# Kernel optimization log

Measured on AMD Instinct MI355X. Metric: run time of the kernel, lower is better.

The kernel has to match this reference:

```python
import jax, jax.numpy as jnp
import numpy as np

EPS = 1e-5

def conv1d(x, w, b):
    # Keras Conv1D, channels_last, padding='same'. x: [B,L,Cin], w: [K,Cin,Cout]
    y = jax.lax.conv_general_dilated(x, w, window_strides=(1,), padding='SAME',
                                     dimension_numbers=('NWC', 'WIO', 'NWC'))
    return y + b

def rmsnorm(x, w):
    return x * jax.lax.rsqrt(jnp.mean(jnp.square(x), axis=-1, keepdims=True) + EPS) * w

def setup_inputs() -> dict:
    key = jax.random.key(0)
    ks = jax.random.split(key, 12)
    B, L, D, S = 4, 4096, 512, 16
    D2 = 2 * D
    def w(k, shape, scale=0.02):
        return (jax.random.normal(k, shape, jnp.float32) * scale)
    return {
        'x': jax.random.normal(ks[0], (B, L, D), jnp.float32),
        'norm_w': jnp.ones((D,), jnp.float32),
        'inp_w': w(ks[1], (3, D, D2)),  'inp_b': jnp.zeros((D2,), jnp.float32),
        'conv_w': w(ks[2], (3, D2, D2)), 'conv_b': jnp.zeros((D2,), jnp.float32),
        'cl_w': w(ks[3], (3, D2, D2)),   'cl_b': jnp.zeros((D2,), jnp.float32),
        'fc1_w': w(ks[4], (3, D2, D2)),  'fc1_b': jnp.zeros((D2,), jnp.float32),
        'fc2_w': w(ks[5], (3, D2, S)),   'fc2_b': jnp.zeros((S,), jnp.float32),
        'fc3_w': w(ks[6], (3, D2, S)),   'fc3_b': jnp.zeros((S,), jnp.float32),
        'A': w(ks[7], (D2, S), 0.1),
        'res_w': w(ks[8], (3, D, D2)),   'res_b': jnp.zeros((D2,), jnp.float32),
        'out_w': w(ks[9], (3, D2, D)),   'out_b': jnpp if False else jnp.zeros((D,), jnp.float32),
    }

def s6(x, fc1_w, fc1_b, fc2_w, fc2_b, fc3_w, fc3_b, A):
    # Original: dB = delta[...,None]*B[:,:,None,:]; dA = exp(delta[...,None]*A);
    # h = dA * zeros + x[...,None] * dB  ==  x[...,None] * dB  (dA term is exactly 0)
    # y = einsum('bln,bldn->bld', C, h) = x * delta * sum_n(C*B)
    Bm = conv1d(x, fc2_w, fc2_b)            # [B,L,n]
    Cm = conv1d(x, fc3_w, fc3_b)            # [B,L,n]
    delta = jax.nn.softplus(conv1d(x, fc1_w, fc1_b))  # [B,L,2d]
    cb = jnp.einsum('bln,bln->bl', Cm, Bm)  # [B,L]
    return x * delta * cb[..., None]        # [B,L,2d]

def reference(x, norm_w, inp_w, inp_b, conv_w, conv_b, cl_w, cl_b,
              fc1_w, fc1_b, fc2_w, fc2_b, fc3_w, fc3_b, A,
              res_w, res_b, out_w, out_b):
    xn = rmsnorm(x, norm_w)
    x_proj = conv1d(xn, inp_w, inp_b)
    x_conv = jax.nn.swish(conv1d(x_proj, conv_w, conv_b))
    x_conv_out = conv1d(x_conv, cl_w, cl_b)
    x_ssm = s6(x_conv_out, fc1_w, fc1_b, fc2_w, fc2_b, fc3_w, fc3_b, A)
    x_res = jax.nn.swish(conv1d(xn, res_w, res_b))
    return conv1d(x_ssm * x_res, out_w, out_b)
```

## Files before the change

### kernel.cpp

```cpp
#include <hip/hip_runtime.h>
#include <hip/hip_fp16.h>

typedef _Float16 f16;
typedef _Float16 half8  __attribute__((ext_vector_type(8)));
typedef _Float16 half4v __attribute__((ext_vector_type(4)));
typedef _Float16 half2v __attribute__((ext_vector_type(2)));
typedef float    floatx4 __attribute__((ext_vector_type(4)));

constexpr int SEQ  = 4096;
constexpr int SEQP = 4098;

__device__ __forceinline__ void dma16(const void* g, char* ldsBase, unsigned off) {
  __builtin_amdgcn_global_load_lds(
      (const __attribute__((address_space(1))) void*)g,
      (__attribute__((address_space(3))) void*)(ldsBase + off),
      16, 0, 0);
}

template <int EPI>
__global__ __launch_bounds__(256, 2)
void gemm_k(const f16* __restrict__ A, const f16* __restrict__ Wt,
            const float* __restrict__ bias, void* __restrict__ Cp,
            int K, int lda, long batchStrideA,
            int ldc, long batchStrideC, int rowOff)
{
  __shared__ f16 lds[8192];
  char* ldsB = (char*)lds;

  const int tid  = threadIdx.x;
  const int lane = tid & 63;
  const int wv   = tid >> 6;
  const int quad = lane >> 4;
  const int lr   = lane & 15;
  const int w_row = wv >> 1, w_col = wv & 1;

  const int r0 = blockIdx.x * 128;
  const int n0 = blockIdx.y * 128;
  const int b  = r0 >> 12;
  const int l0 = r0 & (SEQ - 1);

  const f16* Ab = A + (long)b * batchStrideA + (long)l0 * lda;

  const int c0 = tid, c1 = tid + 256;
  const f16* gA0 = Ab + (long)(c0 >> 2) * lda + (c0 & 3) * 8;
  const f16* gA1 = Ab + (long)(c1 >> 2) * lda + (c1 & 3) * 8;
  const f16* gB0 = Wt + (long)(n0 + (c0 >> 2)) * K + (c0 & 3) * 8;
  const f16* gB1 = Wt + (long)(n0 + (c1 >> 2)) * K + (c1 & 3) * 8;
  const unsigned la0 = wv * 1024;
  const unsigned la1 = 4096  + wv * 1024;
  const unsigned lb0 = 8192  + wv * 1024;
  const unsigned lb1 = 12288 + wv * 1024;

  floatx4 acc[4][4];
#pragma unroll
  for (int mi = 0; mi < 4; mi++)
#pragma unroll
    for (int ni = 0; ni < 4; ni++) acc[mi][ni] = (floatx4){0.f, 0.f, 0.f, 0.f};

  for (int k0 = 0; k0 < K; k0 += 32) {
    __syncthreads();
    dma16(gA0 + k0, ldsB, la0);
    dma16(gA1 + k0, ldsB, la1);
    dma16(gB0 + k0, ldsB, lb0);
    dma16(gB1 + k0, ldsB, lb1);
    __syncthreads();

    half8 af[4], bf[4];
#pragma unroll
    for (int mi = 0; mi < 4; mi++)
      af[mi] = *(const half8*)&lds[(w_row * 64 + mi * 16 + lr) * 32 + quad * 8];
#pragma unroll
    for (int ni = 0; ni < 4; ni++)
      bf[ni] = *(const half8*)&lds[4096 + (w_col * 64 + ni * 16 + lr) * 32 + quad * 8];

#pragma unroll
    for (int mi = 0; mi < 4; mi++)
#pragma unroll
      for (int ni = 0; ni < 4; ni++)
        acc[mi][ni] = __builtin_amdgcn_mfma_f32_16x16x32_f16(af[mi], bf[ni], acc[mi][ni], 0, 0, 0);
  }

  const int colBase = n0 + w_col * 64 + lr;
  float bv[4];
#pragma unroll
  for (int ni = 0; ni < 4; ni++) bv[ni] = bias[colBase + ni * 16];

  const long cbb = (long)b * batchStrideC;
#pragma unroll
  for (int mi = 0; mi < 4; mi++) {
#pragma unroll
    for (int i = 0; i < 4; i++) {
      const int rl = w_row * 64 + mi * 16 + quad * 4 + i;
      const long rowFlat = cbb + (long)(l0 + rl + rowOff) * ldc;
#pragma unroll
      for (int ni = 0; ni < 4; ni++) {
        float v = acc[mi][ni][i] + bv[ni];
        if (EPI == 1) v = v / (1.f + expf(-v));
        if (EPI == 2) ((float*)Cp)[rowFlat + colBase + ni * 16] = v;
        else          ((f16*)Cp)[rowFlat + colBase + ni * 16] = (f16)v;
      }
    }
  }
}

__global__ __launch_bounds__(256)
void wt_transpose(const float* __restrict__ w, f16* __restrict__ wt, int K, int N)
{
  __shared__ float tile[32][33];
  const int kt = blockIdx.x * 32, nt = blockIdx.y * 32;
  const int tx = threadIdx.x & 31, ty = threadIdx.x >> 5;
#pragma unroll
  for (int i = 0; i < 32; i += 8)
    tile[ty + i][tx] = w[(long)(kt + ty + i) * N + nt + tx];
  __syncthreads();
#pragma unroll
  for (int i = 0; i < 32; i += 8)
    wt[(long)(nt + ty + i) * K + kt + tx] = (f16)tile[tx][ty + i];
}

__global__ void fc23_build(const float* __restrict__ fc2, const float* __restrict__ fc3,
                           f16* __restrict__ wt)
{
  int idx = blockIdx.x * 256 + threadIdx.x;
  int n = idx / 3072, k = idx - n * 3072;
  float v = 0.f;
  if (n < 16)      v = fc2[k * 16 + n];
  else if (n < 32) v = fc3[k * 16 + n - 16];
  wt[idx] = (f16)v;
}

__global__ void fc23_bias(const float* __restrict__ b2, const float* __restrict__ b3,
                          float* __restrict__ bo)
{
  int t = threadIdx.x;
  if (t < 128) bo[t] = t < 16 ? b2[t] : (t < 32 ? b3[t - 16] : 0.f);
}

__global__ void zero_pads(f16* xn, f16* xproj, f16* xconv, f16* xco)
{
  int b = blockIdx.x >> 1, e = blockIdx.x & 1;
  f16* base; int C;
  switch (blockIdx.y) {
    case 0:  base = xn;    C = 512;  break;
    case 1:  base = xproj; C = 1024; break;
    case 2:  base = xconv; C = 1024; break;
    default: base = xco;   C = 1024; break;
  }
  long p = e ? (SEQP - 1) : 0;
  f16* row = base + ((long)b * SEQP + p) * C;
  for (int c = threadIdx.x; c < C; c += 256) row[c] = (f16)0;
}

__global__ __launch_bounds__(256)
void rmsnorm_k(const float* __restrict__ x, const float* __restrict__ nw,
               f16* __restrict__ xn)
{
  const int row = blockIdx.x;
  const int b = row >> 12, l = row & (SEQ - 1);
  const int t = threadIdx.x;
  float2 v = ((const float2*)(x + (long)row * 512))[t];
  float ss = v.x * v.x + v.y * v.y;
#pragma unroll
  for (int o = 32; o > 0; o >>= 1) ss += __shfl_down(ss, o, 64);
  __shared__ float sred[4];
  if ((t & 63) == 0) sred[t >> 6] = ss;
  __syncthreads();
  float tot = sred[0] + sred[1] + sred[2] + sred[3];
  float rs = rsqrtf(tot * (1.f / 512.f) + 1e-5f);
  float2 w = ((const float2*)nw)[t];
  half2v o2;
  o2.x = (f16)(v.x * rs * w.x);
  o2.y = (f16)(v.y * rs * w.y);
  ((half2v*)(xn + ((long)b * SEQP + l + 1) * 512))[t] = o2;
}

__global__ __launch_bounds__(256)
void combine_k(const f16* __restrict__ delta_pre, const f16* __restrict__ xco_pad,
               const f16* __restrict__ bmcm, const f16* __restrict__ xres,
               f16* __restrict__ prod_pad)
{
  const int row = blockIdx.x;
  const int b = row >> 12, l = row & (SEQ - 1);
  const int t = threadIdx.x;
  __shared__ float cb_s;
  if (t < 16) {
    float bmv = (float)bmcm[(long)row * 128 + t];
    float cmv = (float)bmcm[(long)row * 128 + 16 + t];
    float p = bmv * cmv;
#pragma unroll
    for (int o = 8; o > 0; o >>= 1) p += __shfl_down(p, o, 64);
    if (t == 0) cb_s = p;
  }
  __syncthreads();
  const float cb = cb_s;
  const long urow = (long)row * 1024;
  const long prow = ((long)b * SEQP + l + 1) * 1024;
  half4v dp = ((const half4v*)(delta_pre + urow))[t];
  half4v xc = ((const half4v*)(xco_pad + prow))[t];
  half4v xr = ((const half4v*)(xres + urow))[t];
  half4v o;
#pragma unroll
  for (int j = 0; j < 4; j++) {
    float d  = (float)dp[j];
    float sp = d > 20.f ? d : log1pf(expf(d));
    o[j] = (f16)((float)xc[j] * sp * cb * (float)xr[j]);
  }
  ((half4v*)(prod_pad + prow))[t] = o;
}

extern "C" void kernel_launch(void* const* d_in, const int* in_sizes, int n_in,
                              void* d_out, int out_size, void* d_ws, size_t ws_size,
                              hipStream_t stream)
{
  const float* x      = (const float*)d_in[0];
  const float* norm_w = (const float*)d_in[1];
  const float* inp_w  = (const float*)d_in[2];
  const float* inp_b  = (const float*)d_in[3];
  const float* conv_w = (const float*)d_in[4];
  const float* conv_b = (const float*)d_in[5];
  const float* cl_w   = (const float*)d_in[6];
  const float* cl_b   = (const float*)d_in[7];
  const float* fc1_w  = (const float*)d_in[8];
  const float* fc1_b  = (const float*)d_in[9];
  const float* fc2_w  = (const float*)d_in[10];
  const float* fc2_b  = (const float*)d_in[11];
  const float* fc3_w  = (const float*)d_in[12];
  const float* fc3_b  = (const float*)d_in[13];
  const float* res_w  = (const float*)d_in[15];
  const float* res_b  = (const float*)d_in[16];
  const float* out_w  = (const float*)d_in[17];
  const float* out_b  = (const float*)d_in[18];

  char* ws = (char*)d_ws;
  size_t off = 0;
  auto alloc = [&](size_t bytes) -> char* {
    char* p = ws + off; off += (bytes + 511) & ~(size_t)511; return p;
  };
  f16* Wt_inp   = (f16*)alloc(1024ull * 1536 * 2);
  f16* Wt_conv  = (f16*)alloc(1024ull * 3072 * 2);
  f16* Wt_cl    = (f16*)alloc(1024ull * 3072 * 2);
  f16* Wt_fc1   = (f16*)alloc(1024ull * 3072 * 2);
  f16* Wt_fc23  = (f16*)alloc(128ull  * 3072 * 2);
  f16* Wt_res   = (f16*)alloc(1024ull * 1536 * 2);
  f16* Wt_out   = (f16*)alloc(512ull  * 3072 * 2);
  float* b_fc23 = (float*)alloc(128 * 4);
  f16* xn_pad    = (f16*)alloc(4ull * SEQP * 512  * 2);
  f16* xproj_pad = (f16*)alloc(4ull * SEQP * 1024 * 2);
  f16* xconv_pad = (f16*)alloc(4ull * SEQP * 1024 * 2);
  f16* xco_pad   = (f16*)alloc(4ull * SEQP * 1024 * 2);
  f16* bmcm      = (f16*)alloc(16384ull * 128  * 2);
  f16* xres      = (f16*)alloc(16384ull * 1024 * 2);

  wt_transpose<<<dim3(1536 / 32, 1024 / 32), 256, 0, stream>>>(inp_w,  Wt_inp,  1536, 1024);
  wt_transpose<<<dim3(3072 / 32, 1024 / 32), 256, 0, stream>>>(conv_w, Wt_conv, 3072, 1024);
  wt_transpose<<<dim3(3072 / 32, 1024 / 32), 256, 0, stream>>>(cl_w,   Wt_cl,   3072, 1024);
  wt_transpose<<<dim3(3072 / 32, 1024 / 32), 256, 0, stream>>>(fc1_w,  Wt_fc1,  3072, 1024);
  wt_transpose<<<dim3(1536 / 32, 1024 / 32), 256, 0, stream>>>(res_w,  Wt_res,  1536, 1024);
  wt_transpose<<<dim3(3072 / 32,  512 / 32), 256, 0, stream>>>(out_w,  Wt_out,  3072, 512);
  fc23_build<<<1536, 256, 0, stream>>>(fc2_w, fc3_w, Wt_fc23);
  fc23_bias<<<1, 128, 0, stream>>>(fc2_b, fc3_b, b_fc23);
  zero_pads<<<dim3(8, 4), 256, 0, stream>>>(xn_pad, xproj_pad, xconv_pad, xco_pad);

  rmsnorm_k<<<16384, 256, 0, stream>>>(x, norm_w, xn_pad);

  gemm_k<0><<<dim3(128, 8), 256, 0, stream>>>(xn_pad, Wt_inp, inp_b, xproj_pad,
      1536, 512, (long)SEQP * 512, 1024, (long)SEQP * 1024, 1);
  gemm_k<1><<<dim3(128, 8), 256, 0, stream>>>(xproj_pad, Wt_conv, conv_b, xconv_pad,
      3072, 1024, (long)SEQP * 1024, 1024, (long)SEQP * 1024, 1);
  gemm_k<0><<<dim3(128, 8), 256, 0, stream>>>(xconv_pad, Wt_cl, cl_b, xco_pad,
      3072, 1024, (long)SEQP * 1024, 1024, (long)SEQP * 1024, 1);
  f16* delta_pre = xconv_pad;
  gemm_k<0><<<dim3(128, 8), 256, 0, stream>>>(xco_pad, Wt_fc1, fc1_b, delta_pre,
      3072, 1024, (long)SEQP * 1024, 1024, (long)SEQ * 1024, 0);
  gemm_k<0><<<dim3(128, 1), 256, 0, stream>>>(xco_pad, Wt_fc23, b_fc23, bmcm,
      3072, 1024, (long)SEQP * 1024, 128, (long)SEQ * 128, 0);
  gemm_k<1><<<dim3(128, 8), 256, 0, stream>>>(xn_pad, Wt_res, res_b, xres,
      1536, 512, (long)SEQP * 512, 1024, (long)SEQ * 1024, 0);
  f16* prod_pad = xproj_pad;
  combine_k<<<16384, 256, 0, stream>>>(delta_pre, xco_pad, bmcm, xres, prod_pad);
  gemm_k<2><<<dim3(128, 4), 256, 0, stream>>>(prod_pad, Wt_out, out_b, d_out,
      3072, 1024, (long)SEQP * 1024, 512, (long)SEQ * 512, 0);
}
```

Baseline: 858.7 us.

## Fuse combine into res GEMM epilogue, merge fc1/fc23 GEMMs, swizzle LDS

```diff
diff --git a/kernel.cpp b/kernel.cpp
--- a/kernel.cpp
+++ b/kernel.cpp
@@ -3,7 +3,6 @@
 
 typedef _Float16 f16;
 typedef _Float16 half8  __attribute__((ext_vector_type(8)));
-typedef _Float16 half4v __attribute__((ext_vector_type(4)));
 typedef _Float16 half2v __attribute__((ext_vector_type(2)));
 typedef float    floatx4 __attribute__((ext_vector_type(4)));
 
@@ -21,6 +20,8 @@
 __global__ __launch_bounds__(256, 2)
 void gemm_k(const f16* __restrict__ A, const f16* __restrict__ Wt,
             const float* __restrict__ bias, void* __restrict__ Cp,
+            void* __restrict__ Cp2, const f16* __restrict__ Edelta,
+            const f16* __restrict__ Exco, const float* __restrict__ Ecb,
             int K, int lda, long batchStrideA,
             int ldc, long batchStrideC, int rowOff)
 {
@@ -41,11 +42,13 @@
 
   const f16* Ab = A + (long)b * batchStrideA + (long)l0 * lda;
 
-  const int c0 = tid, c1 = tid + 256;
-  const f16* gA0 = Ab + (long)(c0 >> 2) * lda + (c0 & 3) * 8;
-  const f16* gA1 = Ab + (long)(c1 >> 2) * lda + (c1 & 3) * 8;
-  const f16* gB0 = Wt + (long)(n0 + (c0 >> 2)) * K + (c0 & 3) * 8;
-  const f16* gB1 = Wt + (long)(n0 + (c1 >> 2)) * K + (c1 & 3) * 8;
+  const int s0 = tid, s1 = tid + 256;
+  const int r0s = s0 >> 2, c0s = ((s0 & 3) ^ ((s0 >> 3) & 3)) * 8;
+  const int r1s = s1 >> 2, c1s = ((s1 & 3) ^ ((s1 >> 3) & 3)) * 8;
+  const f16* gA0 = Ab + (long)r0s * lda + c0s;
+  const f16* gA1 = Ab + (long)r1s * lda + c1s;
+  const f16* gB0 = Wt + (long)(n0 + r0s) * K + c0s;
+  const f16* gB1 = Wt + (long)(n0 + r1s) * K + c1s;
   const unsigned la0 = wv * 1024;
   const unsigned la1 = 4096  + wv * 1024;
   const unsigned lb0 = 8192  + wv * 1024;
@@ -56,6 +59,8 @@
   for (int mi = 0; mi < 4; mi++)
 #pragma unroll
     for (int ni = 0; ni < 4; ni++) acc[mi][ni] = (floatx4){0.f, 0.f, 0.f, 0.f};
+
+  const int swz = (quad ^ ((lr >> 1) & 3)) * 8;
 
   for (int k0 = 0; k0 < K; k0 += 32) {
     __syncthreads();
@@ -68,10 +73,10 @@
     half8 af[4], bf[4];
 #pragma unroll
     for (int mi = 0; mi < 4; mi++)
-      af[mi] = *(const half8*)&lds[(w_row * 64 + mi * 16 + lr) * 32 + quad * 8];
+      af[mi] = *(const half8*)&lds[(w_row * 64 + mi * 16 + lr) * 32 + swz];
 #pragma unroll
     for (int ni = 0; ni < 4; ni++)
-      bf[ni] = *(const half8*)&lds[4096 + (w_col * 64 + ni * 16 + lr) * 32 + quad * 8];
+      bf[ni] = *(const half8*)&lds[4096 + (w_col * 64 + ni * 16 + lr) * 32 + swz];
 
 #pragma unroll
     for (int mi = 0; mi < 4; mi++)
@@ -92,30 +97,62 @@
     for (int i = 0; i < 4; i++) {
       const int rl = w_row * 64 + mi * 16 + quad * 4 + i;
       const long rowFlat = cbb + (long)(l0 + rl + rowOff) * ldc;
+      const int rg = r0 + rl;
 #pragma unroll
       for (int ni = 0; ni < 4; ni++) {
+        const int c = colBase + ni * 16;
         float v = acc[mi][ni][i] + bv[ni];
-        if (EPI == 1) v = v / (1.f + expf(-v));
-        if (EPI == 2) ((float*)Cp)[rowFlat + colBase + ni * 16] = v;
-        else          ((f16*)Cp)[rowFlat + colBase + ni * 16] = (f16)v;
+        if (EPI == 0) {
+          ((f16*)Cp)[rowFlat + c] = (f16)v;
+        } else if (EPI == 1) {
+          v = v / (1.f + expf(-v));
+          ((f16*)Cp)[rowFlat + c] = (f16)v;
+        } else if (EPI == 2) {
+          ((float*)Cp)[rowFlat + c] = v;
+        } else if (EPI == 3) {
+          v = v / (1.f + expf(-v));
+          float d  = (float)Edelta[(long)rg * 1024 + c];
+          float sp = d > 20.f ? d : log1pf(expf(d));
+          float xc = (float)Exco[rowFlat + c];
+          ((f16*)Cp)[rowFlat + c] = (f16)(xc * sp * Ecb[rg] * v);
+        } else {
+          if (c < 1024)      ((f16*)Cp)[rowFlat + c] = (f16)v;
+          else if (c < 1056) ((f16*)Cp2)[(long)rg * 32 + (c - 1024)] = (f16)v;
+        }
       }
     }
   }
 }
 
 __global__ __launch_bounds__(256)
-void wt_transpose(const float* __restrict__ w, f16* __restrict__ wt, int K, int N)
-{
+void wt_all(const float* __restrict__ s0, const float* __restrict__ s1,
+            const float* __restrict__ s2, const float* __restrict__ s3,
+            const float* __restrict__ s4, const float* __restrict__ s5,
+            f16* d0, f16* d1, f16* d2, f16* d3, f16* d4, f16* d5)
+{
+  const float* src; f16* dst; int K, N;
+  switch (blockIdx.y) {
+    case 0:  src = s0; dst = d0; K = 1536; N = 1024; break;
+    case 1:  src = s1; dst = d1; K = 3072; N = 1024; break;
+    case 2:  src = s2; dst = d2; K = 3072; N = 1024; break;
+    case 3:  src = s3; dst = d3; K = 3072; N = 1024; break;
+    case 4:  src = s4; dst = d4; K = 1536; N = 1024; break;
+    default: src = s5; dst = d5; K = 3072; N = 512;  break;
+  }
+  const int ktiles = K >> 5;
+  const int t = blockIdx.x;
+  if (t >= ktiles * (N >> 5)) return;
+  const int kt = (t % ktiles) * 32, nt = (t / ktiles) * 32;
+
   __shared__ float tile[32][33];
-  const int kt = blockIdx.x * 32, nt = blockIdx.y * 32;
   const int tx = threadIdx.x & 31, ty = threadIdx.x >> 5;
 #pragma unroll
   for (int i = 0; i < 32; i += 8)
-    tile[ty + i][tx] = w[(long)(kt + ty + i) * N + nt + tx];
+    tile[ty + i][tx] = src[(long)(kt + ty + i) * N + nt + tx];
   __syncthreads();
 #pragma unroll
   for (int i = 0; i < 32; i += 8)
-    wt[(long)(nt + ty + i) * K + kt + tx] = (f16)tile[tx][ty + i];
+    dst[(long)(nt + ty + i) * K + kt + tx] = (f16)tile[tx][ty + i];
 }
 
 __global__ void fc23_build(const float* __restrict__ fc2, const float* __restrict__ fc3,
@@ -129,11 +166,16 @@
   wt[idx] = (f16)v;
 }
 
-__global__ void fc23_bias(const float* __restrict__ b2, const float* __restrict__ b3,
-                          float* __restrict__ bo)
-{
-  int t = threadIdx.x;
-  if (t < 128) bo[t] = t < 16 ? b2[t] : (t < 32 ? b3[t - 16] : 0.f);
+__global__ void bias_build(const float* __restrict__ b1, const float* __restrict__ b2,
+                           const float* __restrict__ b3, float* __restrict__ bo)
+{
+  int t = blockIdx.x * 256 + threadIdx.x;
+  if (t >= 1152) return;
+  float v = 0.f;
+  if (t < 1024)      v = b1[t];
+  else if (t < 1040) v = b2[t - 1024];
+  else if (t < 1056) v = b3[t - 1040];
+  bo[t] = v;
 }
 
 __global__ void zero_pads(f16* xn, f16* xproj, f16* xconv, f16* xco)
@@ -175,37 +217,16 @@
 }
 
 __global__ __launch_bounds__(256)
-void combine_k(const f16* __restrict__ delta_pre, const f16* __restrict__ xco_pad,
-               const f16* __restrict__ bmcm, const f16* __restrict__ xres,
-               f16* __restrict__ prod_pad)
-{
-  const int row = blockIdx.x;
-  const int b = row >> 12, l = row & (SEQ - 1);
-  const int t = threadIdx.x;
-  __shared__ float cb_s;
-  if (t < 16) {
-    float bmv = (float)bmcm[(long)row * 128 + t];
-    float cmv = (float)bmcm[(long)row * 128 + 16 + t];
-    float p = bmv * cmv;
-#pragma unroll
-    for (int o = 8; o > 0; o >>= 1) p += __shfl_down(p, o, 64);
-    if (t == 0) cb_s = p;
-  }
-  __syncthreads();
-  const float cb = cb_s;
-  const long urow = (long)row * 1024;
-  const long prow = ((long)b * SEQP + l + 1) * 1024;
-  half4v dp = ((const half4v*)(delta_pre + urow))[t];
-  half4v xc = ((const half4v*)(xco_pad + prow))[t];
-  half4v xr = ((const half4v*)(xres + urow))[t];
-  half4v o;
-#pragma unroll
-  for (int j = 0; j < 4; j++) {
-    float d  = (float)dp[j];
-    float sp = d > 20.f ? d : log1pf(expf(d));
-    o[j] = (f16)((float)xc[j] * sp * cb * (float)xr[j]);
-  }
-  ((half4v*)(prod_pad + prow))[t] = o;
+void cb_k(const f16* __restrict__ bmcm, float* __restrict__ cb)
+{
+  int r = blockIdx.x * 256 + threadIdx.x;
+  const half8* p = (const half8*)(bmcm + (long)r * 32);
+  half8 b0 = p[0], b1 = p[1], c0 = p[2], c1 = p[3];
+  float s = 0.f;
+#pragma unroll
+  for (int j = 0; j < 8; j++)
+    s += (float)b0[j] * (float)c0[j] + (float)b1[j] * (float)c1[j];
+  cb[r] = s;
 }
 
 extern "C" void kernel_launch(void* const* d_in, const int* in_sizes, int n_in,
@@ -239,45 +260,44 @@
   f16* Wt_inp   = (f16*)alloc(1024ull * 1536 * 2);
   f16* Wt_conv  = (f16*)alloc(1024ull * 3072 * 2);
   f16* Wt_cl    = (f16*)alloc(1024ull * 3072 * 2);
-  f16* Wt_fc1   = (f16*)alloc(1024ull * 3072 * 2);
-  f16* Wt_fc23  = (f16*)alloc(128ull  * 3072 * 2);
+  f16* Wt_fc1x  = (f16*)alloc(1152ull * 3072 * 2);
   f16* Wt_res   = (f16*)alloc(1024ull * 1536 * 2);
   f16* Wt_out   = (f16*)alloc(512ull  * 3072 * 2);
-  float* b_fc23 = (float*)alloc(128 * 4);
+  float* b_fc1x = (float*)alloc(1152 * 4);
   f16* xn_pad    = (f16*)alloc(4ull * SEQP * 512  * 2);
   f16* xproj_pad = (f16*)alloc(4ull * SEQP * 1024 * 2);
   f16* xconv_pad = (f16*)alloc(4ull * SEQP * 1024 * 2);
   f16* xco_pad   = (f16*)alloc(4ull * SEQP * 1024 * 2);
-  f16* bmcm      = (f16*)alloc(16384ull * 128  * 2);
-  f16* xres      = (f16*)alloc(16384ull * 1024 * 2);
-
-  wt_transpose<<<dim3(1536 / 32, 1024 / 32), 256, 0, stream>>>(inp_w,  Wt_inp,  1536, 1024);
-  wt_transpose<<<dim3(3072 / 32, 1024 / 32), 256, 0, stream>>>(conv_w, Wt_conv, 3072, 1024);
-  wt_transpose<<<dim3(3072 / 32, 1024 / 32), 256, 0, stream>>>(cl_w,   Wt_cl,   3072, 1024);
-  wt_transpose<<<dim3(3072 / 32, 1024 / 32), 256, 0, stream>>>(fc1_w,  Wt_fc1,  3072, 1024);
-  wt_transpose<<<dim3(1536 / 32, 1024 / 32), 256, 0, stream>>>(res_w,  Wt_res,  1536, 1024);
-  wt_transpose<<<dim3(3072 / 32,  512 / 32), 256, 0, stream>>>(out_w,  Wt_out,  3072, 512);
-  fc23_build<<<1536, 256, 0, stream>>>(fc2_w, fc3_w, Wt_fc23);
-  fc23_bias<<<1, 128, 0, stream>>>(fc2_b, fc3_b, b_fc23);
+  f16* bmcm      = (f16*)alloc(16384ull * 32 * 2);
+  float* cb      = (float*)alloc(16384ull * 4);
+
+  wt_all<<<dim3(3072, 6), 256, 0, stream>>>(inp_w, conv_w, cl_w, fc1_w, res_w, out_w,
+                                            Wt_inp, Wt_conv, Wt_cl, Wt_fc1x, Wt_res, Wt_out);
+  fc23_build<<<1536, 256, 0, stream>>>(fc2_w, fc3_w, Wt_fc1x + 1024ull * 3072);
+  bias_build<<<5, 256, 0, stream>>>(fc1_b, fc2_b, fc3_b, b_fc1x);
   zero_pads<<<dim3(8, 4), 256, 0, stream>>>(xn_pad, xproj_pad, xconv_pad, xco_pad);
 
   rmsnorm_k<<<16384, 256, 0, stream>>>(x, norm_w, xn_pad);
 
   gemm_k<0><<<dim3(128, 8), 256, 0, stream>>>(xn_pad, Wt_inp, inp_b, xproj_pad,
+      nullptr, nullptr, nullptr, nullptr,
       1536, 512, (long)SEQP * 512, 1024, (long)SEQP * 1024, 1);
   gemm_k<1><<<dim3(128, 8), 256, 0, stream>>>(xproj_pad, Wt_conv, conv_b, xconv_pad,
+      nullptr, nullptr, nullptr, nullptr,
       3072, 1024, (long)SEQP * 1024, 1024, (long)SEQP * 1024, 1);
   gemm_k<0><<<dim3(128, 8), 256, 0, stream>>>(xconv_pad, Wt_cl, cl_b, xco_pad,
+      nullptr, nullptr, nullptr, nullptr,
       3072, 1024, (long)SEQP * 1024, 1024, (long)SEQP * 1024, 1);
   f16* delta_pre = xconv_pad;
-  gemm_k<0><<<dim3(128, 8), 256, 0, stream>>>(xco_pad, Wt_fc1, fc1_b, delta_pre,
+  gemm_k<4><<<dim3(128, 9), 256, 0, stream>>>(xco_pad, Wt_fc1x, b_fc1x, delta_pre,
+      bmcm, nullptr, nullptr, nullptr,
       3072, 1024, (long)SEQP * 1024, 1024, (long)SEQ * 1024, 0);
-  gemm_k<0><<<dim3(128, 1), 256, 0, stream>>>(xco_pad, Wt_fc23, b_fc23, bmcm,
-      3072, 1024, (long)SEQP * 1024, 128, (long)SEQ * 128, 0);
-  gemm_k<1><<<dim3(128, 8), 256, 0, stream>>>(xn_pad, Wt_res, res_b, xres,
-      1536, 512, (long)SEQP * 512, 1024, (long)SEQ * 1024, 0);
+  cb_k<<<64, 256, 0, stream>>>(bmcm, cb);
   f16* prod_pad = xproj_pad;
-  combine_k<<<16384, 256, 0, stream>>>(delta_pre, xco_pad, bmcm, xres, prod_pad);
+  gemm_k<3><<<dim3(128, 8), 256, 0, stream>>>(xn_pad, Wt_res, res_b, prod_pad,
+      nullptr, delta_pre, xco_pad, cb,
+      1536, 512, (long)SEQP * 512, 1024, (long)SEQP * 1024, 1);
   gemm_k<2><<<dim3(128, 4), 256, 0, stream>>>(prod_pad, Wt_out, out_b, d_out,
+      nullptr, nullptr, nullptr, nullptr,
       3072, 1024, (long)SEQP * 1024, 512, (long)SEQ * 512, 0);
 }
```

Result: no change. 863.7 us (+0.6%).

## Deepen GEMM K-step with swizzled LDS, merge inp/res GEMMs, split-K fc23

Applied to the files above, without the earlier changes.

```diff
diff --git a/kernel.cpp b/kernel.cpp
--- a/kernel.cpp
+++ b/kernel.cpp
@@ -21,10 +21,11 @@
 __global__ __launch_bounds__(256, 2)
 void gemm_k(const f16* __restrict__ A, const f16* __restrict__ Wt,
             const float* __restrict__ bias, void* __restrict__ Cp,
-            int K, int lda, long batchStrideA,
-            int ldc, long batchStrideC, int rowOff)
-{
-  __shared__ f16 lds[8192];
+            void* __restrict__ Cp2,
+            int kSlice, int lda, long bsA, int ldb,
+            int ldc, long bsC, int rowOff)
+{
+  __shared__ f16 lds[16384];
   char* ldsB = (char*)lds;
 
   const int tid  = threadIdx.x;
@@ -38,18 +39,13 @@
   const int n0 = blockIdx.y * 128;
   const int b  = r0 >> 12;
   const int l0 = r0 & (SEQ - 1);
-
-  const f16* Ab = A + (long)b * batchStrideA + (long)l0 * lda;
-
-  const int c0 = tid, c1 = tid + 256;
-  const f16* gA0 = Ab + (long)(c0 >> 2) * lda + (c0 & 3) * 8;
-  const f16* gA1 = Ab + (long)(c1 >> 2) * lda + (c1 & 3) * 8;
-  const f16* gB0 = Wt + (long)(n0 + (c0 >> 2)) * K + (c0 & 3) * 8;
-  const f16* gB1 = Wt + (long)(n0 + (c1 >> 2)) * K + (c1 & 3) * 8;
-  const unsigned la0 = wv * 1024;
-  const unsigned la1 = 4096  + wv * 1024;
-  const unsigned lb0 = 8192  + wv * 1024;
-  const unsigned lb1 = 12288 + wv * 1024;
+  const int kBeg = blockIdx.z * kSlice;
+
+  const int trow   = tid >> 3;
+  const int tchunk = ((tid & 7) ^ ((tid >> 3) & 7)) * 8;
+  const f16* gA = A + (long)b * bsA + (long)(l0 + trow) * lda + kBeg + tchunk;
+  const f16* gB = Wt + (long)(n0 + trow) * ldb + kBeg + tchunk;
+  const long stepA = 32l * lda, stepB = 32l * ldb;
 
   floatx4 acc[4][4];
 #pragma unroll
@@ -57,65 +53,104 @@
 #pragma unroll
     for (int ni = 0; ni < 4; ni++) acc[mi][ni] = (floatx4){0.f, 0.f, 0.f, 0.f};
 
-  for (int k0 = 0; k0 < K; k0 += 32) {
+  const int colx = (quad ^ (lr & 7)) * 8;
+
+  for (int k0 = 0; k0 < kSlice; k0 += 64) {
     __syncthreads();
-    dma16(gA0 + k0, ldsB, la0);
-    dma16(gA1 + k0, ldsB, la1);
-    dma16(gB0 + k0, ldsB, lb0);
-    dma16(gB1 + k0, ldsB, lb1);
+#pragma unroll
+    for (int j = 0; j < 4; j++) {
+      dma16(gA + k0 + j * stepA, ldsB,         j * 4096 + wv * 1024);
+      dma16(gB + k0 + j * stepB, ldsB, 16384 + j * 4096 + wv * 1024);
+    }
     __syncthreads();
 
-    half8 af[4], bf[4];
-#pragma unroll
-    for (int mi = 0; mi < 4; mi++)
-      af[mi] = *(const half8*)&lds[(w_row * 64 + mi * 16 + lr) * 32 + quad * 8];
-#pragma unroll
-    for (int ni = 0; ni < 4; ni++)
-      bf[ni] = *(const half8*)&lds[4096 + (w_col * 64 + ni * 16 + lr) * 32 + quad * 8];
-
-#pragma unroll
-    for (int mi = 0; mi < 4; mi++)
+#pragma unroll
+    for (int s = 0; s < 2; s++) {
+      const int cs = colx ^ (s * 32);
+      half8 af[4], bf[4];
+#pragma unroll
+      for (int mi = 0; mi < 4; mi++)
+        af[mi] = *(const half8*)&lds[(w_row * 64 + mi * 16 + lr) * 64 + cs];
 #pragma unroll
       for (int ni = 0; ni < 4; ni++)
-        acc[mi][ni] = __builtin_amdgcn_mfma_f32_16x16x32_f16(af[mi], bf[ni], acc[mi][ni], 0, 0, 0);
+        bf[ni] = *(const half8*)&lds[8192 + (w_col * 64 + ni * 16 + lr) * 64 + cs];
+#pragma unroll
+      for (int mi = 0; mi < 4; mi++)
+#pragma unroll
+        for (int ni = 0; ni < 4; ni++)
+          acc[mi][ni] = __builtin_amdgcn_mfma_f32_16x16x32_f16(af[mi], bf[ni], acc[mi][ni], 0, 0, 0);
+    }
   }
 
   const int colBase = n0 + w_col * 64 + lr;
   float bv[4];
 #pragma unroll
-  for (int ni = 0; ni < 4; ni++) bv[ni] = bias[colBase + ni * 16];
-
-  const long cbb = (long)b * batchStrideC;
+  for (int ni = 0; ni < 4; ni++)
+    bv[ni] = (EPI == 6 && blockIdx.z != 0) ? 0.f : bias[colBase + ni * 16];
+
+  const long cbb = (long)b * bsC;
 #pragma unroll
   for (int mi = 0; mi < 4; mi++) {
 #pragma unroll
     for (int i = 0; i < 4; i++) {
       const int rl = w_row * 64 + mi * 16 + quad * 4 + i;
       const long rowFlat = cbb + (long)(l0 + rl + rowOff) * ldc;
+      const int rg = r0 + rl;
 #pragma unroll
       for (int ni = 0; ni < 4; ni++) {
+        const int c = colBase + ni * 16;
         float v = acc[mi][ni][i] + bv[ni];
-        if (EPI == 1) v = v / (1.f + expf(-v));
-        if (EPI == 2) ((float*)Cp)[rowFlat + colBase + ni * 16] = v;
-        else          ((f16*)Cp)[rowFlat + colBase + ni * 16] = (f16)v;
+        if (EPI == 0) {
+          ((f16*)Cp)[rowFlat + c] = (f16)v;
+        } else if (EPI == 1) {
+          v = v / (1.f + expf(-v));
+          ((f16*)Cp)[rowFlat + c] = (f16)v;
+        } else if (EPI == 2) {
+          ((float*)Cp)[rowFlat + c] = v;
+        } else if (EPI == 5) {
+          if (c < 1024) {
+            ((f16*)Cp)[cbb + (long)(l0 + rl + 1) * 1024 + c] = (f16)v;
+          } else {
+            v = v / (1.f + expf(-v));
+            ((f16*)Cp2)[(long)rg * 1024 + (c - 1024)] = (f16)v;
+          }
+        } else {
+          if (c < 32) atomicAdd((float*)Cp + (long)rg * 32 + c, v);
+        }
       }
     }
   }
 }
 
 __global__ __launch_bounds__(256)
-void wt_transpose(const float* __restrict__ w, f16* __restrict__ wt, int K, int N)
-{
+void wt_all(const float* __restrict__ s0, const float* __restrict__ s1,
+            const float* __restrict__ s2, const float* __restrict__ s3,
+            const float* __restrict__ s4, const float* __restrict__ s5,
+            f16* d0, f16* d1, f16* d2, f16* d3, f16* d4, f16* d5)
+{
+  const float* src; f16* dst; int K, N;
+  switch (blockIdx.y) {
+    case 0:  src = s0; dst = d0; K = 1536; N = 1024; break;
+    case 1:  src = s1; dst = d1; K = 3072; N = 1024; break;
+    case 2:  src = s2; dst = d2; K = 3072; N = 1024; break;
+    case 3:  src = s3; dst = d3; K = 3072; N = 1024; break;
+    case 4:  src = s4; dst = d4; K = 1536; N = 1024; break;
+    default: src = s5; dst = d5; K = 3072; N = 512;  break;
+  }
+  const int ktiles = K >> 5;
+  const int t = blockIdx.x;
+  if (t >= ktiles * (N >> 5)) return;
+  const int kt = (t % ktiles) * 32, nt = (t / ktiles) * 32;
+
   __shared__ float tile[32][33];
-  const int kt = blockIdx.x * 32, nt = blockIdx.y * 32;
   const int tx = threadIdx.x & 31, ty = threadIdx.x >> 5;
 #pragma unroll
   for (int i = 0; i < 32; i += 8)
-    tile[ty + i][tx] = w[(long)(kt + ty + i) * N + nt + tx];
+    tile[ty + i][tx] = src[(long)(kt + ty + i) * N + nt + tx];
   __syncthreads();
 #pragma unroll
   for (int i = 0; i < 32; i += 8)
-    wt[(long)(nt + ty + i) * K + kt + tx] = (f16)tile[tx][ty + i];
+    dst[(long)(nt + ty + i) * K + kt + tx] = (f16)tile[tx][ty + i];
 }
 
 __global__ void fc23_build(const float* __restrict__ fc2, const float* __restrict__ fc3,
@@ -129,11 +164,17 @@
   wt[idx] = (f16)v;
 }
 
-__global__ void fc23_bias(const float* __restrict__ b2, const float* __restrict__ b3,
-                          float* __restrict__ bo)
-{
-  int t = threadIdx.x;
-  if (t < 128) bo[t] = t < 16 ? b2[t] : (t < 32 ? b3[t - 16] : 0.f);
+__global__ void bias_build(const float* __restrict__ bi, const float* __restrict__ br,
+                           const float* __restrict__ b2, const float* __restrict__ b3,
+                           float* __restrict__ b_inpres, float* __restrict__ b_fc23)
+{
+  int t = blockIdx.x * 256 + threadIdx.x;
+  if (t < 1024)      b_inpres[t] = bi[t];
+  else if (t < 2048) b_inpres[t] = br[t - 1024];
+  else if (t < 2176) {
+    int u = t - 2048;
+    b_fc23[u] = u < 16 ? b2[u] : (u < 32 ? b3[u - 16] : 0.f);
+  }
 }
 
 __global__ void zero_pads(f16* xn, f16* xproj, f16* xconv, f16* xco)
@@ -149,6 +190,11 @@
   long p = e ? (SEQP - 1) : 0;
   f16* row = base + ((long)b * SEQP + p) * C;
   for (int c = threadIdx.x; c < C; c += 256) row[c] = (f16)0;
+}
+
+__global__ void zero_f32(float4* p)
+{
+  p[blockIdx.x * 256 + threadIdx.x] = (float4){0.f, 0.f, 0.f, 0.f};
 }
 
 __global__ __launch_bounds__(256)
@@ -176,7 +222,7 @@
 
 __global__ __launch_bounds__(256)
 void combine_k(const f16* __restrict__ delta_pre, const f16* __restrict__ xco_pad,
-               const f16* __restrict__ bmcm, const f16* __restrict__ xres,
+               const float* __restrict__ bmcmF, const f16* __restrict__ xres,
                f16* __restrict__ prod_pad)
 {
   const int row = blockIdx.x;
@@ -184,9 +230,7 @@
   const int t = threadIdx.x;
   __shared__ float cb_s;
   if (t < 16) {
-    float bmv = (float)bmcm[(long)row * 128 + t];
-    float cmv = (float)bmcm[(long)row * 128 + 16 + t];
-    float p = bmv * cmv;
+    float p = bmcmF[(long)row * 32 + t] * bmcmF[(long)row * 32 + 16 + t];
 #pragma unroll
     for (int o = 8; o > 0; o >>= 1) p += __shfl_down(p, o, 64);
     if (t == 0) cb_s = p;
@@ -236,48 +280,43 @@
   auto alloc = [&](size_t bytes) -> char* {
     char* p = ws + off; off += (bytes + 511) & ~(size_t)511; return p;
   };
-  f16* Wt_inp   = (f16*)alloc(1024ull * 1536 * 2);
-  f16* Wt_conv  = (f16*)alloc(1024ull * 3072 * 2);
-  f16* Wt_cl    = (f16*)alloc(1024ull * 3072 * 2);
-  f16* Wt_fc1   = (f16*)alloc(1024ull * 3072 * 2);
-  f16* Wt_fc23  = (f16*)alloc(128ull  * 3072 * 2);
-  f16* Wt_res   = (f16*)alloc(1024ull * 1536 * 2);
-  f16* Wt_out   = (f16*)alloc(512ull  * 3072 * 2);
-  float* b_fc23 = (float*)alloc(128 * 4);
+  f16* Wt_inpres = (f16*)alloc(2048ull * 1536 * 2);
+  f16* Wt_conv   = (f16*)alloc(1024ull * 3072 * 2);
+  f16* Wt_cl     = (f16*)alloc(1024ull * 3072 * 2);
+  f16* Wt_fc1    = (f16*)alloc(1024ull * 3072 * 2);
+  f16* Wt_fc23   = (f16*)alloc(128ull  * 3072 * 2);
+  f16* Wt_out    = (f16*)alloc(512ull  * 3072 * 2);
+  float* b_inpres = (float*)alloc(2048 * 4);
+  float* b_fc23   = (float*)alloc(128 * 4);
   f16* xn_pad    = (f16*)alloc(4ull * SEQP * 512  * 2);
   f16* xproj_pad = (f16*)alloc(4ull * SEQP * 1024 * 2);
   f16* xconv_pad = (f16*)alloc(4ull * SEQP * 1024 * 2);
   f16* xco_pad   = (f16*)alloc(4ull * SEQP * 1024 * 2);
-  f16* bmcm      = (f16*)alloc(16384ull * 128  * 2);
   f16* xres      = (f16*)alloc(16384ull * 1024 * 2);
-
-  wt_transpose<<<dim3(1536 / 32, 1024 / 32), 256, 0, stream>>>(inp_w,  Wt_inp,  1536, 1024);
-  wt_transpose<<<dim3(3072 / 32, 1024 / 32), 256, 0, stream>>>(conv_w, Wt_conv, 3072, 1024);
-  wt_transpose<<<dim3(3072 / 32, 1024 / 32), 256, 0, stream>>>(cl_w,   Wt_cl,   3072, 1024);
-  wt_transpose<<<dim3(3072 / 32, 1024 / 32), 256, 0, stream>>>(fc1_w,  Wt_fc1,  3072, 1024);
-  wt_transpose<<<dim3(1536 / 32, 1024 / 32), 256, 0, stream>>>(res_w,  Wt_res,  1536, 1024);
-  wt_transpose<<<dim3(3072 / 32,  512 / 32), 256, 0, stream>>>(out_w,  Wt_out,  3072, 512);
+  float* bmcmF   = (float*)alloc(16384ull * 32 * 4);
+
+  wt_all<<<dim3(3072, 6), 256, 0, stream>>>(inp_w, conv_w, cl_w, fc1_w, res_w, out_w,
+      Wt_inpres, Wt_conv, Wt_cl, Wt_fc1, Wt_inpres + 1024ull * 1536, Wt_out);
   fc23_build<<<1536, 256, 0, stream>>>(fc2_w, fc3_w, Wt_fc23);
-  fc23_bias<<<1, 128, 0, stream>>>(fc2_b, fc3_b, b_fc23);
+  bias_build<<<9, 256, 0, stream>>>(inp_b, res_b, fc2_b, fc3_b, b_inpres, b_fc23);
   zero_pads<<<dim3(8, 4), 256, 0, stream>>>(xn_pad, xproj_pad, xconv_pad, xco_pad);
+  zero_f32<<<512, 256, 0, stream>>>((float4*)bmcmF);
 
   rmsnorm_k<<<16384, 256, 0, stream>>>(x, norm_w, xn_pad);
 
-  gemm_k<0><<<dim3(128, 8), 256, 0, stream>>>(xn_pad, Wt_inp, inp_b, xproj_pad,
-      1536, 512, (long)SEQP * 512, 1024, (long)SEQP * 1024, 1);
-  gemm_k<1><<<dim3(128, 8), 256, 0, stream>>>(xproj_pad, Wt_conv, conv_b, xconv_pad,
-      3072, 1024, (long)SEQP * 1024, 1024, (long)SEQP * 1024, 1);
-  gemm_k<0><<<dim3(128, 8), 256, 0, stream>>>(xconv_pad, Wt_cl, cl_b, xco_pad,
-      3072, 1024, (long)SEQP * 1024, 1024, (long)SEQP * 1024, 1);
+  gemm_k<5><<<dim3(128, 16), 256, 0, stream>>>(xn_pad, Wt_inpres, b_inpres,
+      xproj_pad, xres, 1536, 512, (long)SEQP * 512, 1536, 1024, (long)SEQP * 1024, 1);
+  gemm_k<1><<<dim3(128, 8), 256, 0, stream>>>(xproj_pad, Wt_conv, conv_b,
+      xconv_pad, nullptr, 3072, 1024, (long)SEQP * 1024, 3072, 1024, (long)SEQP * 1024, 1);
+  gemm_k<0><<<dim3(128, 8), 256, 0, stream>>>(xconv_pad, Wt_cl, cl_b,
+      xco_pad, nullptr, 3072, 1024, (long)SEQP * 1024, 3072, 1024, (long)SEQP * 1024, 1);
   f16* delta_pre = xconv_pad;
-  gemm_k<0><<<dim3(128, 8), 256, 0, stream>>>(xco_pad, Wt_fc1, fc1_b, delta_pre,
-      3072, 1024, (long)SEQP * 1024, 1024, (long)SEQ * 1024, 0);
-  gemm_k<0><<<dim3(128, 1), 256, 0, stream>>>(xco_pad, Wt_fc23, b_fc23, bmcm,
-      3072, 1024, (long)SEQP * 1024, 128, (long)SEQ * 128, 0);
-  gemm_k<1><<<dim3(128, 8), 256, 0, stream>>>(xn_pad, Wt_res, res_b, xres,
-      1536, 512, (long)SEQP * 512, 1024, (long)SEQ * 1024, 0);
+  gemm_k<0><<<dim3(128, 8), 256, 0, stream>>>(xco_pad, Wt_fc1, fc1_b,
+      delta_pre, nullptr, 3072, 1024, (long)SEQP * 1024, 3072, 1024, (long)SEQ * 1024, 0);
+  gemm_k<6><<<dim3(128, 1, 8), 256, 0, stream>>>(xco_pad, Wt_fc23, b_fc23,
+      bmcmF, nullptr, 384, 1024, (long)SEQP * 1024, 3072, 32, (long)SEQ * 32, 0);
   f16* prod_pad = xproj_pad;
-  combine_k<<<16384, 256, 0, stream>>>(delta_pre, xco_pad, bmcm, xres, prod_pad);
-  gemm_k<2><<<dim3(128, 4), 256, 0, stream>>>(prod_pad, Wt_out, out_b, d_out,
-      3072, 1024, (long)SEQP * 1024, 512, (long)SEQ * 512, 0);
-}
+  combine_k<<<16384, 256, 0, stream>>>(delta_pre, xco_pad, bmcmF, xres, prod_pad);
+  gemm_k<2><<<dim3(128, 4), 256, 0, stream>>>(prod_pad, Wt_out, out_b,
+      d_out, nullptr, 3072, 1024, (long)SEQP * 1024, 3072, 512, (long)SEQ * 512, 0);
+}
```

Measured after the change: 723.9 us. 1.19x faster.
